# Optimization experiments

Measured on AMD Instinct MI355X. Metric: run time of the kernel, lower is better.

The kernel has to match this reference:

```python
import jax, jax.numpy as jnp
import numpy as np

SEQ, B, IN, H = 256, 64, 512, 1024


def setup_inputs() -> dict:
    key = jax.random.key(0)
    ks = jax.random.split(key, 17)
    s_in = 0.05  # small init to avoid gate saturation
    inp = {"x": jax.random.normal(ks[0], (SEQ, B, IN), dtype=jnp.float32)}
    names = ["f", "i", "o", "c"]
    for j, g in enumerate(names):
        inp[f"W_i{g}"] = jax.random.normal(ks[1 + 4 * j], (H, IN), dtype=jnp.float32) * s_in
        inp[f"b_i{g}"] = jax.random.normal(ks[2 + 4 * j], (H,), dtype=jnp.float32) * s_in
        inp[f"W_h{g}"] = jax.random.normal(ks[3 + 4 * j], (H, H), dtype=jnp.float32) * s_in
        inp[f"b_h{g}"] = jax.random.normal(ks[4 + 4 * j], (H,), dtype=jnp.float32) * s_in
    return inp


def reference(x, W_if, b_if, W_hf, b_hf, W_ii, b_ii, W_hi, b_hi,
              W_io, b_io, W_ho, b_ho, W_ic, b_ic, W_hc, b_hc):
    # Precompute input-to-gate projections for the whole sequence (one big GEMM each)
    xf = jnp.einsum('sbi,hi->sbh', x, W_if) + b_if
    xi = jnp.einsum('sbi,hi->sbh', x, W_ii) + b_ii
    xo = jnp.einsum('sbi,hi->sbh', x, W_io) + b_io
    xc = jnp.einsum('sbi,hi->sbh', x, W_ic) + b_ic

    batch = x.shape[1]
    hidden = W_hf.shape[0]
    h0 = jnp.zeros((batch, hidden), dtype=x.dtype)
    c0 = jnp.zeros((batch, hidden), dtype=x.dtype)

    def step(carry, xs):
        h, c = carry
        xf_t, xi_t, xo_t, xc_t = xs
        f = jax.nn.sigmoid(xf_t + h @ W_hf.T + b_hf)
        i = jax.nn.sigmoid(xi_t + h @ W_hi.T + b_hi)
        o = jax.nn.sigmoid(xo_t + h @ W_ho.T + b_ho)
        g = jnp.tanh(xc_t + h @ W_hc.T + b_hc)
        c_new = f * c + i * g
        h_new = o * jnp.tanh(c_new)
        return (h_new, c_new), h_new

    (h_fin, c_fin), h_seq = jax.lax.scan(step, (h0, c0), (xf, xi, xo, xc))
    # match torch module's (1, B, H) leading layer dim on final states
    return h_seq, h_fin[None], c_fin[None]
```

## Files before the change

### kernel.cpp

```cpp
#include <hip/hip_runtime.h>
#include <hip/hip_bf16.h>

typedef __bf16 bf16_t;
typedef __bf16 bf16x8 __attribute__((ext_vector_type(8)));
typedef float f32x4 __attribute__((ext_vector_type(4)));
typedef int   i32x4 __attribute__((ext_vector_type(4)));

#define SEQLEN 256
#define NBATCH 64
#define INDIM  512
#define HID    1024
#define NBLK   256

#define XF_OFF   0ull
#define WXF_OFF  16777216ull
#define WHF_OFF  20971520ull
#define BS_OFF   29360128ull
#define HSEQ_OFF 29376512ull
#define FLG_OFF  63062016ull
#define SLOT_BYTES 131072ull

__device__ __forceinline__ bf16x8 cvt8(float4 a, float4 b) {
  bf16x8 v;
  v[0] = (bf16_t)a.x; v[1] = (bf16_t)a.y; v[2] = (bf16_t)a.z; v[3] = (bf16_t)a.w;
  v[4] = (bf16_t)b.x; v[5] = (bf16_t)b.y; v[6] = (bf16_t)b.z; v[7] = (bf16_t)b.w;
  return v;
}

__global__ __launch_bounds__(256) void pack_xf_k(const float* __restrict__ x,
                                                 bf16_t* __restrict__ xf) {
  int idx = blockIdx.x * 256 + threadIdx.x;
  int t = idx >> 12;
  int r = idx & 4095;
  int batch = r >> 6, c8 = r & 63;
  const float4* s = (const float4*)(x + ((size_t)t * NBATCH + batch) * INDIM + c8 * 8);
  int kk = c8 >> 2, lhi = c8 & 3;
  int kh = kk >> 3, kkl = kk & 7;
  int bg = batch >> 4, lane = (batch & 15) + 16 * lhi;
  bf16_t* d = xf + (size_t)t * 32768 + (size_t)(((bg * 2 + kh) * 8 + kkl) * 64 + lane) * 8;
  *(bf16x8*)d = cvt8(s[0], s[1]);
}

struct GatePtrs {
  const float* Wi[4];
  const float* bi[4];
  const float* Wh[4];
  const float* bh[4];
};

__global__ __launch_bounds__(256) void pack_w_k(GatePtrs p,
                                                bf16_t* __restrict__ Wxf,
                                                bf16_t* __restrict__ Whf,
                                                float* __restrict__ bsum) {
  int idx = blockIdx.x * 256 + threadIdx.x;
  int row = idx / 192;
  int c   = idx % 192;
  int blk = row >> 5, r32 = row & 31, g = r32 >> 3, jj = r32 & 7;
  int j = blk * 8 + jj;
  int g2 = r32 >> 4, lrow = r32 & 15;
  if (c == 0) bsum[row] = p.bi[g][j] + p.bh[g][j];
  if (c < 64) {
    const float4* s = (const float4*)(p.Wi[g] + (size_t)j * INDIM + c * 8);
    int kk = c >> 2, lane = lrow + 16 * (c & 3);
    *(bf16x8*)(Wxf + (size_t)blk * 16384 + (size_t)((kk * 2 + g2) * 64 + lane) * 8) = cvt8(s[0], s[1]);
  } else {
    int cc = c - 64;
    const float4* s = (const float4*)(p.Wh[g] + (size_t)j * HID + cc * 8);
    int kk = cc >> 2, lane = lrow + 16 * (cc & 3);
    *(bf16x8*)(Whf + (size_t)blk * 32768 + (size_t)((kk * 2 + g2) * 64 + lane) * 8) = cvt8(s[0], s[1]);
  }
}

#define PLDC(dst, ptr, OFF) \
  asm volatile("global_load_dwordx4 %0, %1, off offset:" OFF : "=v"(dst) : "v"(ptr))

__global__ __launch_bounds__(256, 1) void lstm_rec_k(const bf16_t* __restrict__ Whf,
                                                     const bf16_t* __restrict__ Wxf,
                                                     const bf16_t* __restrict__ xf,
                                                     const float* __restrict__ bsum,
                                                     bf16_t* __restrict__ hseq,
                                                     int* __restrict__ flags,
                                                     float* __restrict__ out) {
  const int b = blockIdx.x;
  const int cb = b & 127, bgs = b >> 7;
  const int tid = threadIdx.x;
  const int w = tid >> 6, l = tid & 63;
  const int bhalf = w >> 1, kh = w & 1;
  const int bg = bgs * 2 + bhalf;

  __shared__ bf16_t xwlds[16384];
  __shared__ float  accbuf[2][32][36];
  __shared__ char   ldspad[45056];

  if (tid > 1000000) ((volatile char*)ldspad)[0] = 1;

#pragma unroll
  for (int i = 0; i < 8; ++i)
    __builtin_amdgcn_global_load_lds((const __attribute__((address_space(1))) void*)(Wxf + (size_t)cb * 16384 + (i * 256 + tid) * 8),
                                     (__attribute__((address_space(3))) void*)(xwlds + (i * 256 + tid) * 8),
                                     16, 0, 0);

  i32x4 whr[16][2];
  {
    const char* wb = (const char*)Whf + (size_t)cb * 65536 + (size_t)(kh * 32768) + (size_t)l * 16;
    const char* w0 = wb;          const char* w1 = wb + 4096;
    const char* w2 = wb + 8192;   const char* w3 = wb + 12288;
    const char* w4 = wb + 16384;  const char* w5 = wb + 20480;
    const char* w6 = wb + 24576;  const char* w7 = wb + 28672;
    PLDC(whr[0][0],  w0, "0"); PLDC(whr[0][1],  w0, "1024"); PLDC(whr[1][0],  w0, "2048"); PLDC(whr[1][1],  w0, "3072");
    PLDC(whr[2][0],  w1, "0"); PLDC(whr[2][1],  w1, "1024"); PLDC(whr[3][0],  w1, "2048"); PLDC(whr[3][1],  w1, "3072");
    PLDC(whr[4][0],  w2, "0"); PLDC(whr[4][1],  w2, "1024"); PLDC(whr[5][0],  w2, "2048"); PLDC(whr[5][1],  w2, "3072");
    PLDC(whr[6][0],  w3, "0"); PLDC(whr[6][1],  w3, "1024"); PLDC(whr[7][0],  w3, "2048"); PLDC(whr[7][1],  w3, "3072");
    PLDC(whr[8][0],  w4, "0"); PLDC(whr[8][1],  w4, "1024"); PLDC(whr[9][0],  w4, "2048"); PLDC(whr[9][1],  w4, "3072");
    PLDC(whr[10][0], w5, "0"); PLDC(whr[10][1], w5, "1024"); PLDC(whr[11][0], w5, "2048"); PLDC(whr[11][1], w5, "3072");
    PLDC(whr[12][0], w6, "0"); PLDC(whr[12][1], w6, "1024"); PLDC(whr[13][0], w6, "2048"); PLDC(whr[13][1], w6, "3072");
    PLDC(whr[14][0], w7, "0"); PLDC(whr[14][1], w7, "1024"); PLDC(whr[15][0], w7, "2048"); PLDC(whr[15][1], w7, "3072");
  }
  asm volatile("s_waitcnt vmcnt(0)" ::: "memory");
  __builtin_amdgcn_sched_barrier(0);

  const int eb = tid >> 3, ejj = tid & 7;
  const int gb = bgs * 32 + eb;
  const int j  = cb * 8 + ejj;
  const int p_lane = (gb & 15) + 16 * ((j & 31) >> 3);
  const int p_kkg = j >> 5;
  const size_t pub_off = (size_t)((((gb >> 4) * 2 + (p_kkg >> 4)) * 16 + (p_kkg & 15)) * 64 + p_lane) * 16
                       + (size_t)(j & 7) * 2;
  const float bsF = bsum[cb * 32 + ejj];
  const float bsI = bsum[cb * 32 + 8 + ejj];
  const float bsO = bsum[cb * 32 + 16 + ejj];
  const float bsC = bsum[cb * 32 + 24 + ejj];
  float cs = 0.f;

  const size_t pollbase = (size_t)((bg * 2 + kh) * 16) * 1024 + (size_t)l * 16;
  const char* fbase = (const char*)flags + (size_t)l * 16;

  __syncthreads();

  for (int t = 0; t < SEQLEN; ++t) {
    const char* xp0 = (const char*)xf + (size_t)t * 65536 + (size_t)((bg * 2 + kh) * 8 * 64 + l) * 16;
    const char* xp1 = xp0 + 4096;
    i32x4 xr[8];
    PLDC(xr[0], xp0, "0"); PLDC(xr[1], xp0, "1024"); PLDC(xr[2], xp0, "2048"); PLDC(xr[3], xp0, "3072");
    PLDC(xr[4], xp1, "0"); PLDC(xr[5], xp1, "1024"); PLDC(xr[6], xp1, "2048"); PLDC(xr[7], xp1, "3072");

    if (t) {
      const char* fp = fbase + (size_t)t * 1024;
      i32x4 f;
      for (;;) {
        asm volatile("global_load_dwordx4 %0, %1, off sc0 sc1" : "=v"(f) : "v"(fp));
        asm volatile("s_waitcnt vmcnt(0)" ::: "memory");
        if (!__any((f[0] == 0) | (f[1] == 0) | (f[2] == 0) | (f[3] == 0))) break;
        __builtin_amdgcn_s_sleep(1);
      }
    }
    asm volatile("" ::: "memory");

    const char* q0 = (const char*)hseq + (size_t)t * SLOT_BYTES + pollbase;
    const char* q1 = q0 + 4096;
    const char* q2 = q0 + 8192;
    const char* q3 = q0 + 12288;
    i32x4 hv[16];
    PLDC(hv[0],  q0, "0"); PLDC(hv[1],  q0, "1024"); PLDC(hv[2],  q0, "2048"); PLDC(hv[3],  q0, "3072");
    PLDC(hv[4],  q1, "0"); PLDC(hv[5],  q1, "1024"); PLDC(hv[6],  q1, "2048"); PLDC(hv[7],  q1, "3072");
    PLDC(hv[8],  q2, "0"); PLDC(hv[9],  q2, "1024"); PLDC(hv[10], q2, "2048"); PLDC(hv[11], q2, "3072");
    PLDC(hv[12], q3, "0"); PLDC(hv[13], q3, "1024"); PLDC(hv[14], q3, "2048"); PLDC(hv[15], q3, "3072");

    asm volatile("s_waitcnt vmcnt(16)" ::: "memory");
    __builtin_amdgcn_sched_barrier(0);
    f32x4 acc0 = {}, acc1 = {};
#pragma unroll
    for (int kkl = 0; kkl < 8; ++kkl) {
      const int kk = kh * 8 + kkl;
      bf16x8 xv = __builtin_bit_cast(bf16x8, xr[kkl]);
      bf16x8 w0 = *(const bf16x8*)(xwlds + (size_t)((kk * 2 + 0) * 64 + l) * 8);
      bf16x8 w1 = *(const bf16x8*)(xwlds + (size_t)((kk * 2 + 1) * 64 + l) * 8);
      acc0 = __builtin_amdgcn_mfma_f32_16x16x32_bf16(xv, w0, acc0, 0, 0, 0);
      acc1 = __builtin_amdgcn_mfma_f32_16x16x32_bf16(xv, w1, acc1, 0, 0, 0);
    }

    asm volatile("s_waitcnt vmcnt(0)" ::: "memory");
    __builtin_amdgcn_sched_barrier(0);
#pragma unroll
    for (int kkl = 0; kkl < 16; ++kkl) {
      bf16x8 hf = __builtin_bit_cast(bf16x8, hv[kkl]);
      acc0 = __builtin_amdgcn_mfma_f32_16x16x32_bf16(hf, __builtin_bit_cast(bf16x8, whr[kkl][0]), acc0, 0, 0, 0);
      acc1 = __builtin_amdgcn_mfma_f32_16x16x32_bf16(hf, __builtin_bit_cast(bf16x8, whr[kkl][1]), acc1, 0, 0, 0);
    }

    *(f32x4*)&accbuf[kh][l & 15][bhalf * 16 + (l >> 4) * 4]        = acc0;
    *(f32x4*)&accbuf[kh][16 + (l & 15)][bhalf * 16 + (l >> 4) * 4] = acc1;
    __syncthreads();

    float hval;
    {
      float pf = bsF + accbuf[0][ejj][eb]      + accbuf[1][ejj][eb];
      float pi = bsI + accbuf[0][8 + ejj][eb]  + accbuf[1][8 + ejj][eb];
      float po = bsO + accbuf[0][16 + ejj][eb] + accbuf[1][16 + ejj][eb];
      float pc = bsC + accbuf[0][24 + ejj][eb] + accbuf[1][24 + ejj][eb];
      float fg = 1.f / (1.f + __expf(-pf));
      float ig = 1.f / (1.f + __expf(-pi));
      float og = 1.f / (1.f + __expf(-po));
      float e2 = __expf(-2.f * fabsf(pc));
      float gg = __builtin_copysignf((1.f - e2) / (1.f + e2), pc);
      cs = fg * cs + ig * gg;
      float e2c = __expf(-2.f * fabsf(cs));
      float th = __builtin_copysignf((1.f - e2c) / (1.f + e2c), cs);
      hval = og * th;

      unsigned int my = (unsigned int)__builtin_bit_cast(unsigned short, (bf16_t)hval);
      unsigned int other = __shfl_xor(my, 1);
      if (!(tid & 1)) {
        unsigned int pk = my | (other << 16);
        unsigned int* hd = (unsigned int*)((char*)hseq + (size_t)(t + 1) * SLOT_BYTES + pub_off);
        __hip_atomic_store(hd, pk, __ATOMIC_RELAXED, __HIP_MEMORY_SCOPE_AGENT);
      }
    }

    __syncthreads();
    if (t < SEQLEN - 1 && tid == 0)
      __hip_atomic_store(&flags[(t + 1) * NBLK + b], 1, __ATOMIC_RELAXED, __HIP_MEMORY_SCOPE_AGENT);

    out[((size_t)t * NBATCH + gb) * HID + j] = hval;
    if (t == SEQLEN - 1) {
      out[(size_t)SEQLEN * NBATCH * HID + (size_t)gb * HID + j] = hval;
      out[(size_t)SEQLEN * NBATCH * HID + (size_t)NBATCH * HID + (size_t)gb * HID + j] = cs;
    }
  }
}

extern "C" void kernel_launch(void* const* d_in, const int* in_sizes, int n_in,
                              void* d_out, int out_size, void* d_ws, size_t ws_size,
                              hipStream_t stream) {
  (void)in_sizes; (void)n_in; (void)out_size; (void)ws_size;
  char* ws = (char*)d_ws;
  bf16_t* xf   = (bf16_t*)(ws + XF_OFF);
  bf16_t* Wxf  = (bf16_t*)(ws + WXF_OFF);
  bf16_t* Whf  = (bf16_t*)(ws + WHF_OFF);
  float*  bs   = (float*)(ws + BS_OFF);
  bf16_t* hseq = (bf16_t*)(ws + HSEQ_OFF);
  int*    flg  = (int*)(ws + FLG_OFF);

  const float* x = (const float*)d_in[0];
  GatePtrs p;
  for (int g = 0; g < 4; ++g) {
    p.Wi[g] = (const float*)d_in[1 + 4 * g];
    p.bi[g] = (const float*)d_in[2 + 4 * g];
    p.Wh[g] = (const float*)d_in[3 + 4 * g];
    p.bh[g] = (const float*)d_in[4 + 4 * g];
  }

  pack_xf_k<<<4096, 256, 0, stream>>>(x, xf);
  pack_w_k<<<3072, 256, 0, stream>>>(p, Wxf, Whf, bs);
  hipMemsetAsync(flg, 0, 257 * NBLK * 4, stream);
  hipMemsetAsync(hseq, 0, SLOT_BYTES, stream);
  lstm_rec_k<<<NBLK, 256, 0, stream>>>(Whf, Wxf, xf, bs, hseq, flg, (float*)d_out);
}
```

Before: 736.8 us.

## Overlap flag polling with input MFMAs and defer h output to finalize kernel

The first flag poll is now issued alongside the x-projection loads, so the x·Wx MFMAs run while the step-dependency flag is in flight. Only after that does the kernel spin, if still needed, and then load the shared h slot. Per-step fp32 stores of h are removed from the recurrent loop. A separate finalize kernel afterwards converts the bf16 hseq slots into h_seq and h_fin, which takes global store traffic off the serial critical path. The flags for step 0 are preset to 1 so the poll needs no branch, and the unused LDS padding array is dropped. In exchange, the h outputs are now bf16-rounded values rather than the fp32 results, and one extra kernel launch is added.

After: 749.7 us. About the same (+1.8%).

```diff
diff --git a/kernel.cpp b/kernel.cpp
--- a/kernel.cpp
+++ b/kernel.cpp
@@ -19,6 +19,7 @@
 #define HSEQ_OFF 29376512ull
 #define FLG_OFF  63062016ull
 #define SLOT_BYTES 131072ull
+#define SLOT_ELEMS 65536
 
 __device__ __forceinline__ bf16x8 cvt8(float4 a, float4 b) {
   bf16x8 v;
@@ -71,6 +72,25 @@
   }
 }
 
+__global__ __launch_bounds__(256) void finalize_k(const bf16_t* __restrict__ hseq,
+                                                  float* __restrict__ out) {
+  int idx = blockIdx.x * 256 + threadIdx.x;
+  int c = idx & 127;
+  int batch = (idx >> 7) & 63;
+  int t = idx >> 13;
+  int slot = (t < 256) ? (t + 1) : 256;
+  int j0 = c * 8;
+  int kkg = j0 >> 5;
+  int sub = (j0 & 31) >> 3;
+  int lane = (batch & 15) + 16 * sub;
+  int bg2 = (batch >> 4) * 2 + (kkg >> 4);
+  const bf16_t* src = hseq + (size_t)slot * SLOT_ELEMS + (size_t)((bg2 * 16 + (kkg & 15)) * 64 + lane) * 8;
+  bf16x8 v = *(const bf16x8*)src;
+  float* d = out + ((size_t)t * NBATCH + batch) * HID + j0;
+  *(float4*)d       = make_float4((float)v[0], (float)v[1], (float)v[2], (float)v[3]);
+  *(float4*)(d + 4) = make_float4((float)v[4], (float)v[5], (float)v[6], (float)v[7]);
+}
+
 #define PLDC(dst, ptr, OFF) \
   asm volatile("global_load_dwordx4 %0, %1, off offset:" OFF : "=v"(dst) : "v"(ptr))
 
@@ -90,9 +110,6 @@
 
   __shared__ bf16_t xwlds[16384];
   __shared__ float  accbuf[2][32][36];
-  __shared__ char   ldspad[45056];
-
-  if (tid > 1000000) ((volatile char*)ldspad)[0] = 1;
 
 #pragma unroll
   for (int i = 0; i < 8; ++i)
@@ -143,30 +160,11 @@
     i32x4 xr[8];
     PLDC(xr[0], xp0, "0"); PLDC(xr[1], xp0, "1024"); PLDC(xr[2], xp0, "2048"); PLDC(xr[3], xp0, "3072");
     PLDC(xr[4], xp1, "0"); PLDC(xr[5], xp1, "1024"); PLDC(xr[6], xp1, "2048"); PLDC(xr[7], xp1, "3072");
-
-    if (t) {
-      const char* fp = fbase + (size_t)t * 1024;
-      i32x4 f;
-      for (;;) {
-        asm volatile("global_load_dwordx4 %0, %1, off sc0 sc1" : "=v"(f) : "v"(fp));
-        asm volatile("s_waitcnt vmcnt(0)" ::: "memory");
-        if (!__any((f[0] == 0) | (f[1] == 0) | (f[2] == 0) | (f[3] == 0))) break;
-        __builtin_amdgcn_s_sleep(1);
-      }
-    }
-    asm volatile("" ::: "memory");
-
-    const char* q0 = (const char*)hseq + (size_t)t * SLOT_BYTES + pollbase;
-    const char* q1 = q0 + 4096;
-    const char* q2 = q0 + 8192;
-    const char* q3 = q0 + 12288;
-    i32x4 hv[16];
-    PLDC(hv[0],  q0, "0"); PLDC(hv[1],  q0, "1024"); PLDC(hv[2],  q0, "2048"); PLDC(hv[3],  q0, "3072");
-    PLDC(hv[4],  q1, "0"); PLDC(hv[5],  q1, "1024"); PLDC(hv[6],  q1, "2048"); PLDC(hv[7],  q1, "3072");
-    PLDC(hv[8],  q2, "0"); PLDC(hv[9],  q2, "1024"); PLDC(hv[10], q2, "2048"); PLDC(hv[11], q2, "3072");
-    PLDC(hv[12], q3, "0"); PLDC(hv[13], q3, "1024"); PLDC(hv[14], q3, "2048"); PLDC(hv[15], q3, "3072");
-
-    asm volatile("s_waitcnt vmcnt(16)" ::: "memory");
+    const char* fp = fbase + (size_t)t * 1024;
+    i32x4 f;
+    asm volatile("global_load_dwordx4 %0, %1, off sc0 sc1" : "=v"(f) : "v"(fp));
+
+    asm volatile("s_waitcnt vmcnt(1)" ::: "memory");
     __builtin_amdgcn_sched_barrier(0);
     f32x4 acc0 = {}, acc1 = {};
 #pragma unroll
@@ -181,6 +179,25 @@
 
     asm volatile("s_waitcnt vmcnt(0)" ::: "memory");
     __builtin_amdgcn_sched_barrier(0);
+    while (__any((f[0] == 0) | (f[1] == 0) | (f[2] == 0) | (f[3] == 0))) {
+      __builtin_amdgcn_s_sleep(1);
+      asm volatile("global_load_dwordx4 %0, %1, off sc0 sc1" : "=v"(f) : "v"(fp));
+      asm volatile("s_waitcnt vmcnt(0)" ::: "memory");
+      __builtin_amdgcn_sched_barrier(0);
+    }
+
+    const char* q0 = (const char*)hseq + (size_t)t * SLOT_BYTES + pollbase;
+    const char* q1 = q0 + 4096;
+    const char* q2 = q0 + 8192;
+    const char* q3 = q0 + 12288;
+    i32x4 hv[16];
+    PLDC(hv[0],  q0, "0"); PLDC(hv[1],  q0, "1024"); PLDC(hv[2],  q0, "2048"); PLDC(hv[3],  q0, "3072");
+    PLDC(hv[4],  q1, "0"); PLDC(hv[5],  q1, "1024"); PLDC(hv[6],  q1, "2048"); PLDC(hv[7],  q1, "3072");
+    PLDC(hv[8],  q2, "0"); PLDC(hv[9],  q2, "1024"); PLDC(hv[10], q2, "2048"); PLDC(hv[11], q2, "3072");
+    PLDC(hv[12], q3, "0"); PLDC(hv[13], q3, "1024"); PLDC(hv[14], q3, "2048"); PLDC(hv[15], q3, "3072");
+    asm volatile("s_waitcnt vmcnt(0)" ::: "memory");
+    __builtin_amdgcn_sched_barrier(0);
+
 #pragma unroll
     for (int kkl = 0; kkl < 16; ++kkl) {
       bf16x8 hf = __builtin_bit_cast(bf16x8, hv[kkl]);
@@ -192,7 +209,6 @@
     *(f32x4*)&accbuf[kh][16 + (l & 15)][bhalf * 16 + (l >> 4) * 4] = acc1;
     __syncthreads();
 
-    float hval;
     {
       float pf = bsF + accbuf[0][ejj][eb]      + accbuf[1][ejj][eb];
       float pi = bsI + accbuf[0][8 + ejj][eb]  + accbuf[1][8 + ejj][eb];
@@ -206,7 +222,7 @@
       cs = fg * cs + ig * gg;
       float e2c = __expf(-2.f * fabsf(cs));
       float th = __builtin_copysignf((1.f - e2c) / (1.f + e2c), cs);
-      hval = og * th;
+      float hval = og * th;
 
       unsigned int my = (unsigned int)__builtin_bit_cast(unsigned short, (bf16_t)hval);
       unsigned int other = __shfl_xor(my, 1);
@@ -215,17 +231,13 @@
         unsigned int* hd = (unsigned int*)((char*)hseq + (size_t)(t + 1) * SLOT_BYTES + pub_off);
         __hip_atomic_store(hd, pk, __ATOMIC_RELAXED, __HIP_MEMORY_SCOPE_AGENT);
       }
+      if (t == SEQLEN - 1)
+        out[(size_t)SEQLEN * NBATCH * HID + (size_t)NBATCH * HID + (size_t)gb * HID + j] = cs;
     }
 
     __syncthreads();
     if (t < SEQLEN - 1 && tid == 0)
       __hip_atomic_store(&flags[(t + 1) * NBLK + b], 1, __ATOMIC_RELAXED, __HIP_MEMORY_SCOPE_AGENT);
-
-    out[((size_t)t * NBATCH + gb) * HID + j] = hval;
-    if (t == SEQLEN - 1) {
-      out[(size_t)SEQLEN * NBATCH * HID + (size_t)gb * HID + j] = hval;
-      out[(size_t)SEQLEN * NBATCH * HID + (size_t)NBATCH * HID + (size_t)gb * HID + j] = cs;
-    }
   }
 }
 
@@ -252,7 +264,9 @@
 
   pack_xf_k<<<4096, 256, 0, stream>>>(x, xf);
   pack_w_k<<<3072, 256, 0, stream>>>(p, Wxf, Whf, bs);
-  hipMemsetAsync(flg, 0, 257 * NBLK * 4, stream);
+  hipMemsetAsync(flg, 1, NBLK * 4, stream);
+  hipMemsetAsync(flg + NBLK, 0, 256 * NBLK * 4, stream);
   hipMemsetAsync(hseq, 0, SLOT_BYTES, stream);
   lstm_rec_k<<<NBLK, 256, 0, stream>>>(Whf, Wxf, xf, bs, hseq, flg, (float*)d_out);
-}
+  finalize_k<<<8224, 256, 0, stream>>>(hseq, (float*)d_out);
+}
```
